# Performance work log

Measured on AMD Instinct MI355X. Metric: run time of the kernel, lower is better.

The kernel has to match this reference:

```python
import jax, jax.numpy as jnp
import numpy as np

B, N, C, H, MC, LIE, KD = 2, 2048, 256, 8, 256, 3, 16
DH = C // H

def swish(x):
    return x * jax.nn.sigmoid(x)

def layernorm(x, g, b):
    m = jnp.mean(x, axis=-1, keepdims=True)
    v = jnp.var(x, axis=-1, keepdims=True)
    return (x - m) * jax.lax.rsqrt(v + 1e-5) * g + b

def setup_inputs():
    ks = jax.random.split(jax.random.key(0), 12)
    p = lambda i, shape, s: jax.random.normal(ks[i], shape, jnp.float32) * s
    return dict(
        pairwise_g=jax.random.normal(ks[0], (B, N, N, LIE), jnp.float32),
        x=jax.random.normal(ks[1], (B, N, C), jnp.float32),
        mask=jnp.ones((B, N), dtype=bool),
        ln1_g=jnp.ones((C,), jnp.float32), ln1_b=jnp.zeros((C,), jnp.float32),
        ln2_g=jnp.ones((C,), jnp.float32), ln2_b=jnp.zeros((C,), jnp.float32),
        wn_w1=p(2, (LIE, KD), 0.3), wn_b1=jnp.zeros((KD,), jnp.float32),
        wn_w2=p(3, (KD, KD), 0.3), wn_b2=jnp.zeros((KD,), jnp.float32),
        wn_w3=p(4, (KD, H), 0.3), wn_b3=jnp.zeros((H,), jnp.float32),
        wq=p(5, (C, C), 0.05), bq=jnp.zeros((C,), jnp.float32),
        wk=p(6, (C, C), 0.05), bk=jnp.zeros((C,), jnp.float32),
        in_w=p(7, (C, C), 0.05), in_b=jnp.zeros((C,), jnp.float32),
        out_w=p(8, (C, C), 0.05), out_b=jnp.zeros((C,), jnp.float32),
        mlp_w1=p(9, (C, C), 0.05), mlp_b1=jnp.zeros((C,), jnp.float32),
        mlp_w2=p(10, (C, C), 0.05), mlp_b2=jnp.zeros((C,), jnp.float32),
    )

def _ema(pairwise_g, x, mask, wn_w1, wn_b1, wn_w2, wn_b2, wn_w3, wn_b3,
         wq, bq, wk, bk, in_w, in_b, out_w, out_b):
    b, n, c = x.shape
    # neighbourhood extraction: topk smallest T(3) group distances (mc_samples=MC, fill=1.0)
    dists = jnp.linalg.norm(pairwise_g, axis=-1)                      # (b,n,n)
    dists = jnp.where(mask[:, None, :], dists, jnp.float32(1e8))
    _, idx = jax.lax.top_k(-dists, MC)                                # (b,n,k)
    nbhd_g = jnp.take_along_axis(pairwise_g, idx[..., None], axis=2)  # (b,n,k,LIE)
    nbhd_mask = jnp.take_along_axis(jnp.broadcast_to(mask[:, None, :], (b, n, n)), idx, axis=2)
    # location kernel: MultiheadWeightNet MLP on pairwise group elements -> per-head scalar
    hloc = swish(nbhd_g @ wn_w1 + wn_b1)
    hloc = swish(hloc @ wn_w2 + wn_b2)
    loc = hloc @ wn_w3 + wn_b3                                        # (b,n,k,H)
    # feature kernel: multihead dot product over gathered neighbour keys
    q = (x @ wq + bq).reshape(b, n, H, DH)
    kf = (x @ wk + bk).reshape(b, n, H, DH)
    k_nbhd = jax.vmap(lambda kfb, ib: kfb[ib])(kf, idx)               # (b,n,k,H,DH)
    scores = jnp.einsum('bnhd,bnkhd->bnkh', q, k_nbhd) / jnp.sqrt(jnp.float32(DH))
    pre = jnp.where(nbhd_mask[..., None], loc + scores, jnp.float32(-1e38))
    attn = jax.nn.softmax(pre, axis=2)                                # (b,n,k,H)
    # values; scatter attention into dense (b,n,n,H) exactly as the torch code, then aggregate
    v = (x @ in_w + in_b).reshape(b, n, H, DH)
    BS = jnp.arange(b)[:, None, None]
    NNS = jnp.arange(n)[None, :, None]
    aw = jnp.zeros((b, n, n, H), attn.dtype).at[BS, NNS, idx].set(attn)
    out = jnp.einsum('bnmh,bmhd->bnhd', aw, v).reshape(b, n, c)
    return out @ out_w + out_b

def reference(pairwise_g, x, mask, ln1_g, ln1_b, ln2_g, ln2_b,
              wn_w1, wn_b1, wn_w2, wn_b2, wn_w3, wn_b3,
              wq, bq, wk, bk, in_w, in_b, out_w, out_b,
              mlp_w1, mlp_b1, mlp_w2, mlp_b2):
    # EquivariantTransformerBlock with block_norm='layer_pre'
    x = x + _ema(pairwise_g, layernorm(x, ln1_g, ln1_b), mask,
                 wn_w1, wn_b1, wn_w2, wn_b2, wn_w3, wn_b3,
                 wq, bq, wk, bk, in_w, in_b, out_w, out_b)
    h = layernorm(x, ln2_g, ln2_b)
    x = x + (swish(h @ mlp_w1 + mlp_b1) @ mlp_w2 + mlp_b2)
    return x
```

## Files before the change

### kernel.cpp

```cpp
#include <hip/hip_runtime.h>
#include <hip/hip_bf16.h>

#define Bb 2
#define Nn 2048
#define Cc 256
#define Hh 8
#define MCk 256
#define RT (Bb * Nn)

typedef __hip_bfloat16 bf16;
typedef _Float16 f16;
typedef __fp16 h2v __attribute__((ext_vector_type(2)));
typedef __fp16 h8 __attribute__((ext_vector_type(8)));
typedef float f32x4 __attribute__((ext_vector_type(4)));
typedef float v2f __attribute__((ext_vector_type(2)));

__device__ __forceinline__ float bl(unsigned u) { return __uint_as_float(u << 16); }
__device__ __forceinline__ float bh(unsigned u) { return __uint_as_float(u & 0xFFFF0000u); }
__device__ __forceinline__ h2v bc16(unsigned u) { return __builtin_bit_cast(h2v, u); }
__device__ __forceinline__ unsigned bcu(h2v v) { return __builtin_bit_cast(unsigned, v); }

__device__ __forceinline__ float dot2(h2v a, h2v b, float c) {
  return __builtin_amdgcn_fdot2(a, b, c, false);
}
__device__ __forceinline__ f32x4 mfma16(h8 a, h8 b, f32x4 c) {
  return __builtin_amdgcn_mfma_f32_16x16x32_f16(a, b, c, 0, 0, 0);
}
__device__ __forceinline__ float swish_f(float z) {
  return z * __builtin_amdgcn_rcpf(1.f + __expf(-z));
}

__global__ __launch_bounds__(256) void prep_w(
    const float* __restrict__ w0, const float* __restrict__ w1,
    const float* __restrict__ w2, const float* __restrict__ w3,
    const float* __restrict__ w4, const float* __restrict__ w5,
    f16* __restrict__ out)
{
  __shared__ float tile[32][33];
  const float* ws_[6] = {w0, w1, w2, w3, w4, w5};
  const float* W = ws_[blockIdx.y];
  f16* o = out + (size_t)blockIdx.y * 65536;
  int tn0 = (blockIdx.x & 7) * 32, tk0 = (blockIdx.x >> 3) * 32;
  int tl = threadIdx.x & 31, tg = threadIdx.x >> 5;
#pragma unroll
  for (int r = 0; r < 4; r++) {
    int k = tk0 + tg * 4 + r;
    tile[tg * 4 + r][tl] = W[(size_t)k * 256 + tn0 + tl];
  }
  __syncthreads();
#pragma unroll
  for (int r = 0; r < 4; r++) {
    int n = tn0 + tg * 4 + r;
    o[(size_t)n * 256 + tk0 + tl] = (f16)tile[tl][tg * 4 + r];
  }
}

__global__ __launch_bounds__(256) void ln_kernel(
    const float* __restrict__ x, const float* __restrict__ g,
    const float* __restrict__ b, f16* __restrict__ out)
{
  int wave = threadIdx.x >> 6, lane = threadIdx.x & 63;
  int row = blockIdx.x * 4 + wave;
  const float4 v = reinterpret_cast<const float4*>(x + (size_t)row * Cc)[lane];
  float s  = v.x + v.y + v.z + v.w;
  float s2 = v.x * v.x + v.y * v.y + v.z * v.z + v.w * v.w;
#pragma unroll
  for (int m = 1; m < 64; m <<= 1) {
    s  += __shfl_xor(s, m);
    s2 += __shfl_xor(s2, m);
  }
  float mean = s * (1.0f / Cc);
  float var  = s2 * (1.0f / Cc) - mean * mean;
  float rs   = rsqrtf(var + 1e-5f);
  const float4 gg = reinterpret_cast<const float4*>(g)[lane];
  const float4 bb = reinterpret_cast<const float4*>(b)[lane];
  float ox = (v.x - mean) * rs * gg.x + bb.x;
  float oy = (v.y - mean) * rs * gg.y + bb.y;
  float oz = (v.z - mean) * rs * gg.z + bb.z;
  float ow = (v.w - mean) * rs * gg.w + bb.w;
  uint2 st;
  st.x = bcu(__builtin_amdgcn_cvt_pkrtz(ox, oy));
  st.y = bcu(__builtin_amdgcn_cvt_pkrtz(oz, ow));
  *(uint2*)(out + (size_t)row * Cc + lane * 4) = st;
}

__global__ __launch_bounds__(256) void gemm_qkv_mfma(
    const f16* __restrict__ A,
    const f16* __restrict__ WTq, const float* __restrict__ Bq,
    const f16* __restrict__ WTk, const float* __restrict__ Bk,
    const f16* __restrict__ WTv, const float* __restrict__ Bv,
    f16* __restrict__ outq, f16* __restrict__ outk, bf16* __restrict__ outv)
{
  int wid = threadIdx.x >> 6, lane = threadIdx.x & 63;
  int m0 = (blockIdx.x * 4 + wid) * 16;
  int n0 = blockIdx.y * 32;
  int lm = lane & 15, lk = lane >> 4;
  const h8* Ab = (const h8*)(A + (size_t)(m0 + lm) * 256) + lk;
  const h8* Q0 = (const h8*)(WTq + (size_t)(n0 + lm) * 256) + lk;
  const h8* Q1 = (const h8*)(WTq + (size_t)(n0 + 16 + lm) * 256) + lk;
  const h8* K0 = (const h8*)(WTk + (size_t)(n0 + lm) * 256) + lk;
  const h8* K1 = (const h8*)(WTk + (size_t)(n0 + 16 + lm) * 256) + lk;
  const h8* V0 = (const h8*)(WTv + (size_t)(n0 + lm) * 256) + lk;
  const h8* V1 = (const h8*)(WTv + (size_t)(n0 + 16 + lm) * 256) + lk;
  f32x4 aq0 = {0.f,0.f,0.f,0.f}, aq1 = {0.f,0.f,0.f,0.f};
  f32x4 ak0 = {0.f,0.f,0.f,0.f}, ak1 = {0.f,0.f,0.f,0.f};
  f32x4 av0 = {0.f,0.f,0.f,0.f}, av1 = {0.f,0.f,0.f,0.f};
#pragma unroll
  for (int ks = 0; ks < 8; ks++) {
    h8 a = Ab[ks * 4];
    aq0 = mfma16(a, Q0[ks * 4], aq0);
    aq1 = mfma16(a, Q1[ks * 4], aq1);
    ak0 = mfma16(a, K0[ks * 4], ak0);
    ak1 = mfma16(a, K1[ks * 4], ak1);
    av0 = mfma16(a, V0[ks * 4], av0);
    av1 = mfma16(a, V1[ks * 4], av1);
  }
  const float qs = 0.17677669529663687f;
  float bq0 = Bq[n0 + lm], bq1 = Bq[n0 + 16 + lm];
  float bk0 = Bk[n0 + lm], bk1 = Bk[n0 + 16 + lm];
  float bv0 = Bv[n0 + lm], bv1 = Bv[n0 + 16 + lm];
#pragma unroll
  for (int i = 0; i < 4; i++) {
    size_t row = m0 + lk * 4 + i;
    outq[row * 256 + n0 + lm]      = (f16)((aq0[i] + bq0) * qs);
    outq[row * 256 + n0 + 16 + lm] = (f16)((aq1[i] + bq1) * qs);
    outk[row * 256 + n0 + lm]      = (f16)(ak0[i] + bk0);
    outk[row * 256 + n0 + 16 + lm] = (f16)(ak1[i] + bk1);
    outv[row * 256 + n0 + lm]      = __float2bfloat16(av0[i] + bv0);
    outv[row * 256 + n0 + 16 + lm] = __float2bfloat16(av1[i] + bv1);
  }
}

__global__ __launch_bounds__(256) void select_kernel(
    const float* __restrict__ pg, int* __restrict__ idxout)
{
  __shared__ int idl[4][256];
  int wave = threadIdx.x >> 6, lane = threadIdx.x & 63;
  int row = blockIdx.x * 4 + wave;
  const float* base = pg + (size_t)row * Nn * 3;
  unsigned u[32];
#pragma unroll
  for (int jj = 0; jj < 32; jj++) {
    int col = jj * 64 + lane;
    float g0 = base[col * 3 + 0];
    float g1 = base[col * 3 + 1];
    float g2 = base[col * 3 + 2];
    u[jj] = __float_as_uint(sqrtf(g0 * g0 + g1 * g1 + g2 * g2));
  }
  unsigned T = 0;
  for (int bit = 30; bit >= 0; bit--) {
    unsigned cand = T | (1u << bit);
    int c = 0;
#pragma unroll
    for (int jj = 0; jj < 32; jj++) c += (u[jj] < cand) ? 1 : 0;
#pragma unroll
    for (int m = 1; m < 64; m <<= 1) c += __shfl_xor(c, m);
    if (c <= MCk - 1) T = cand;
  }
  int cl = 0;
#pragma unroll
  for (int jj = 0; jj < 32; jj++) cl += (u[jj] < T) ? 1 : 0;
#pragma unroll
  for (int m = 1; m < 64; m <<= 1) cl += __shfl_xor(cl, m);
  int need = MCk - cl;
  unsigned long long lmask = (1ull << lane) - 1ull;
  int slot = 0;
  for (int jj = 0; jj < 32; jj++) {
    bool eq = (u[jj] == T);
    unsigned long long em = __ballot(eq);
    int ebelow = __popcll(em & lmask);
    bool sel = (u[jj] < T) || (eq && ebelow < need);
    unsigned long long smsk = __ballot(sel);
    if (sel) idl[wave][slot + __popcll(smsk & lmask)] = jj * 64 + lane;
    slot += __popcll(smsk);
    need -= __popcll(em);
    if (need < 0) need = 0;
  }
#pragma unroll
  for (int s = 0; s < 4; s++)
    idxout[(size_t)row * MCk + s * 64 + lane] = idl[wave][s * 64 + lane];
}

__global__ __launch_bounds__(256) void loc_mlp(
    const float* __restrict__ pg, const int* __restrict__ idxb,
    uint4* __restrict__ locout,
    const float* __restrict__ w1, const float* __restrict__ b1,
    const float* __restrict__ w2, const float* __restrict__ b2,
    const float* __restrict__ w3, const float* __restrict__ b3)
{
  __shared__ float wnl[64];
  __shared__ h2v   w2p[128];
  __shared__ float bn2[16];
  __shared__ h2v   w3p[64];
  __shared__ float bn3[8];
  int t = threadIdx.x;
  int row = blockIdx.x;
  for (int i = t; i < 280; i += 256) {
    if (i < 48) {
      wnl[i] = w1[i];
    } else if (i < 64) {
      wnl[i] = b1[i - 48];
    } else if (i < 192) {
      int j = i - 64, i2 = j >> 4, o = j & 15;
      w2p[j] = __builtin_amdgcn_cvt_pkrtz(w2[(2 * i2) * 16 + o], w2[(2 * i2 + 1) * 16 + o]);
    } else if (i < 208) {
      bn2[i - 192] = b2[i - 192];
    } else if (i < 272) {
      int j = i - 208, i2 = j >> 3, o = j & 7;
      w3p[j] = __builtin_amdgcn_cvt_pkrtz(w3[(2 * i2) * 8 + o], w3[(2 * i2 + 1) * 8 + o]);
    } else {
      bn3[i - 272] = b3[i - 272];
    }
  }
  int m = idxb[(size_t)row * 256 + t];
  const float* gsp = pg + ((size_t)row * Nn + m) * 3;
  float g0 = gsp[0], g1 = gsp[1], g2 = gsp[2];
  __syncthreads();
  float h1[16];
#pragma unroll
  for (int o = 0; o < 16; o++) {
    float z = wnl[48 + o] + g0 * wnl[o] + g1 * wnl[16 + o] + g2 * wnl[32 + o];
    h1[o] = swish_f(z);
  }
  h2v hp1[8];
#pragma unroll
  for (int i = 0; i < 8; i++) hp1[i] = __builtin_amdgcn_cvt_pkrtz(h1[2 * i], h1[2 * i + 1]);
  float hh[16];
#pragma unroll
  for (int o = 0; o < 16; o++) {
    float z = bn2[o];
#pragma unroll
    for (int i2 = 0; i2 < 8; i2++) z = dot2(hp1[i2], w2p[i2 * 16 + o], z);
    hh[o] = swish_f(z);
  }
  h2v hp2[8];
#pragma unroll
  for (int i = 0; i < 8; i++) hp2[i] = __builtin_amdgcn_cvt_pkrtz(hh[2 * i], hh[2 * i + 1]);
  float loc[8];
#pragma unroll
  for (int o = 0; o < 8; o++) {
    float z = bn3[o];
#pragma unroll
    for (int i2 = 0; i2 < 8; i2++) z = dot2(hp2[i2], w3p[i2 * 8 + o], z);
    loc[o] = z;
  }
  uint4 lv;
  lv.x = bcu(__builtin_amdgcn_cvt_pkrtz(loc[0], loc[1]));
  lv.y = bcu(__builtin_amdgcn_cvt_pkrtz(loc[2], loc[3]));
  lv.z = bcu(__builtin_amdgcn_cvt_pkrtz(loc[4], loc[5]));
  lv.w = bcu(__builtin_amdgcn_cvt_pkrtz(loc[6], loc[7]));
  locout[(size_t)row * 256 + t] = lv;
}

__global__ __launch_bounds__(256) void attn_kernel(
    const f16* __restrict__ qh, const f16* __restrict__ kh,
    const bf16* __restrict__ vv, const int* __restrict__ idxb,
    const uint4* __restrict__ loc16, f16* __restrict__ out)
{
  __shared__ int   offs[256];
  __shared__ float ps[256 * 9];
  __shared__ float agg[4 * 256];
  __shared__ float red[4][8];
  int t = threadIdx.x;
  int row = blockIdx.x;
  int bidx = row >> 11;
  int g = t >> 5, c = t & 31;

  int m = idxb[(size_t)row * 256 + t];
  offs[t] = (bidx * Nn + m) * 512;
  const uint4 qu = *(const uint4*)((const char*)qh + (size_t)row * 512 + (size_t)c * 16);
  h2v q0 = bc16(qu.x), q1 = bc16(qu.y), q2 = bc16(qu.z), q3 = bc16(qu.w);
  const uint4 lv = loc16[(size_t)row * 256 + t];
  __syncthreads();

  int offr[32];
#pragma unroll
  for (int kk = 0; kk < 32; kk++) offr[kk] = offs[kk * 8 + g];

  const char* kbase = (const char*)kh;
#pragma unroll
  for (int kk = 0; kk < 32; kk++) {
    const uint4 kv = *(const uint4*)(kbase + offr[kk] + c * 16);
    float p = dot2(bc16(kv.x), q0, 0.f);
    p = dot2(bc16(kv.y), q1, p);
    p = dot2(bc16(kv.z), q2, p);
    p = dot2(bc16(kv.w), q3, p);
    p += __shfl_xor(p, 1);
    p += __shfl_xor(p, 2);
    if ((c & 3) == 0) ps[(kk * 8 + g) * 9 + (c >> 2)] = p;
  }
  __syncthreads();

  h2v l01 = bc16(lv.x), l23 = bc16(lv.y), l45 = bc16(lv.z), l67 = bc16(lv.w);
  float pre[8];
  pre[0] = ps[t * 9 + 0] + (float)l01.x;
  pre[1] = ps[t * 9 + 1] + (float)l01.y;
  pre[2] = ps[t * 9 + 2] + (float)l23.x;
  pre[3] = ps[t * 9 + 3] + (float)l23.y;
  pre[4] = ps[t * 9 + 4] + (float)l45.x;
  pre[5] = ps[t * 9 + 5] + (float)l45.y;
  pre[6] = ps[t * 9 + 6] + (float)l67.x;
  pre[7] = ps[t * 9 + 7] + (float)l67.y;
  float mx[8];
#pragma unroll
  for (int h = 0; h < 8; h++) mx[h] = pre[h];
#pragma unroll
  for (int mm = 1; mm < 64; mm <<= 1) {
#pragma unroll
    for (int h = 0; h < 8; h++) mx[h] = fmaxf(mx[h], __shfl_xor(mx[h], mm));
  }
  int wv = t >> 6, ln = t & 63;
  if (ln == 0) {
#pragma unroll
    for (int h = 0; h < 8; h++) red[wv][h] = mx[h];
  }
  __syncthreads();
#pragma unroll
  for (int h = 0; h < 8; h++)
    mx[h] = fmaxf(fmaxf(red[0][h], red[1][h]), fmaxf(red[2][h], red[3][h]));
  float e[8], sm[8];
#pragma unroll
  for (int h = 0; h < 8; h++) { e[h] = __expf(pre[h] - mx[h]); sm[h] = e[h]; }
  __syncthreads();
#pragma unroll
  for (int mm = 1; mm < 64; mm <<= 1) {
#pragma unroll
    for (int h = 0; h < 8; h++) sm[h] += __shfl_xor(sm[h], mm);
  }
  if (ln == 0) {
#pragma unroll
    for (int h = 0; h < 8; h++) red[wv][h] = sm[h];
  }
  __syncthreads();
#pragma unroll
  for (int h = 0; h < 8; h++) {
    float ssum = red[0][h] + red[1][h] + red[2][h] + red[3][h];
    ps[t * 9 + h] = e[h] * __builtin_amdgcn_rcpf(ssum);
  }
  __syncthreads();

  v2f a01 = {0.f, 0.f}, a23 = {0.f, 0.f}, a45 = {0.f, 0.f}, a67 = {0.f, 0.f};
  const char* vbase = (const char*)vv;
#pragma unroll
  for (int kk = 0; kk < 32; kk++) {
    float aw = ps[(kk * 8 + g) * 9 + (c >> 2)];
    v2f awv = {aw, aw};
    uint4 v4 = *(const uint4*)(vbase + offr[kk] + c * 16);
    v2f p0 = {bl(v4.x), bh(v4.x)};
    v2f p1 = {bl(v4.y), bh(v4.y)};
    v2f p2 = {bl(v4.z), bh(v4.z)};
    v2f p3 = {bl(v4.w), bh(v4.w)};
    a01 = __builtin_elementwise_fma(awv, p0, a01);
    a23 = __builtin_elementwise_fma(awv, p1, a23);
    a45 = __builtin_elementwise_fma(awv, p2, a45);
    a67 = __builtin_elementwise_fma(awv, p3, a67);
  }
  float acc[8] = {a01.x, a01.y, a23.x, a23.y, a45.x, a45.y, a67.x, a67.y};
#pragma unroll
  for (int i = 0; i < 8; i++) acc[i] += __shfl_xor(acc[i], 32);
  if ((t & 32) == 0) {
#pragma unroll
    for (int i = 0; i < 8; i++) agg[wv * 256 + c * 8 + i] = acc[i];
  }
  __syncthreads();
  float o = agg[t] + agg[256 + t] + agg[512 + t] + agg[768 + t];
  out[(size_t)row * 256 + t] = (f16)o;
}

__global__ __launch_bounds__(256) void gemm_out_ln(
    const f16* __restrict__ A, const f16* __restrict__ WT,
    const float* __restrict__ bias, const float* __restrict__ xres,
    const float* __restrict__ g, const float* __restrict__ b,
    float* __restrict__ x1, f16* __restrict__ hout)
{
  __shared__ float sred[4][16][2];
  int wid = threadIdx.x >> 6, lane = threadIdx.x & 63;
  int lm = lane & 15, lk = lane >> 4;
  int m0 = blockIdx.x * 16;
  const h8* Ab = (const h8*)(A + (size_t)(m0 + lm) * 256) + lk;
  const h8* Bp[4];
#pragma unroll
  for (int j = 0; j < 4; j++)
    Bp[j] = (const h8*)(WT + (size_t)(wid * 64 + j * 16 + lm) * 256) + lk;
  f32x4 acc[4] = {{0,0,0,0},{0,0,0,0},{0,0,0,0},{0,0,0,0}};
#pragma unroll
  for (int ks = 0; ks < 8; ks++) {
    h8 a = Ab[ks * 4];
#pragma unroll
    for (int j = 0; j < 4; j++) acc[j] = mfma16(a, Bp[j][ks * 4], acc[j]);
  }
  float s[4] = {0,0,0,0}, s2[4] = {0,0,0,0};
#pragma unroll
  for (int j = 0; j < 4; j++) {
    int col = wid * 64 + j * 16 + lm;
    float bc = bias[col];
#pragma unroll
    for (int i = 0; i < 4; i++) {
      size_t row = m0 + lk * 4 + i;
      float y = acc[j][i] + bc + xres[row * 256 + col];
      acc[j][i] = y;
      x1[row * 256 + col] = y;
      s[i] += y; s2[i] += y * y;
    }
  }
#pragma unroll
  for (int mm = 1; mm < 16; mm <<= 1) {
#pragma unroll
    for (int i = 0; i < 4; i++) {
      s[i]  += __shfl_xor(s[i], mm);
      s2[i] += __shfl_xor(s2[i], mm);
    }
  }
  if (lm == 0) {
#pragma unroll
    for (int i = 0; i < 4; i++) {
      sred[wid][lk * 4 + i][0] = s[i];
      sred[wid][lk * 4 + i][1] = s2[i];
    }
  }
  __syncthreads();
#pragma unroll
  for (int i = 0; i < 4; i++) {
    int r = lk * 4 + i;
    float ts  = sred[0][r][0] + sred[1][r][0] + sred[2][r][0] + sred[3][r][0];
    float ts2 = sred[0][r][1] + sred[1][r][1] + sred[2][r][1] + sred[3][r][1];
    float mean = ts * (1.f / 256.f);
    float var  = ts2 * (1.f / 256.f) - mean * mean;
    float rs   = rsqrtf(var + 1e-5f);
    size_t row = m0 + r;
#pragma unroll
    for (int j = 0; j < 4; j++) {
      int col = wid * 64 + j * 16 + lm;
      float hv = (acc[j][i] - mean) * rs * g[col] + b[col];
      hout[row * 256 + col] = (f16)hv;
    }
  }
}

__global__ __launch_bounds__(256) void mlp_fused(
    const f16* __restrict__ A, const f16* __restrict__ WT1,
    const float* __restrict__ b1, const f16* __restrict__ WT2,
    const float* __restrict__ b2, const float* __restrict__ x1,
    float* __restrict__ outp)
{
  __shared__ f16 hl[16 * 272];
  int wid = threadIdx.x >> 6, lane = threadIdx.x & 63;
  int lm = lane & 15, lk = lane >> 4;
  int m0 = blockIdx.x * 16;
  const h8* Ab = (const h8*)(A + (size_t)(m0 + lm) * 256) + lk;
  const h8* B1p[4];
  const h8* B2p[4];
#pragma unroll
  for (int j = 0; j < 4; j++) {
    B1p[j] = (const h8*)(WT1 + (size_t)(wid * 64 + j * 16 + lm) * 256) + lk;
    B2p[j] = (const h8*)(WT2 + (size_t)(wid * 64 + j * 16 + lm) * 256) + lk;
  }
  f32x4 acc[4] = {{0,0,0,0},{0,0,0,0},{0,0,0,0},{0,0,0,0}};
#pragma unroll
  for (int ks = 0; ks < 8; ks++) {
    h8 a = Ab[ks * 4];
#pragma unroll
    for (int j = 0; j < 4; j++) acc[j] = mfma16(a, B1p[j][ks * 4], acc[j]);
  }
#pragma unroll
  for (int j = 0; j < 4; j++) {
    int col = wid * 64 + j * 16 + lm;
    float bc = b1[col];
#pragma unroll
    for (int i = 0; i < 4; i++) {
      float y = acc[j][i] + bc;
      y = y * __builtin_amdgcn_rcpf(1.f + __expf(-y));
      hl[(lk * 4 + i) * 272 + col] = (f16)y;
    }
  }
  __syncthreads();
  f32x4 ac2[4] = {{0,0,0,0},{0,0,0,0},{0,0,0,0},{0,0,0,0}};
#pragma unroll
  for (int ks = 0; ks < 8; ks++) {
    h8 a2 = *(const h8*)&hl[lm * 272 + ks * 32 + lk * 8];
#pragma unroll
    for (int j = 0; j < 4; j++) ac2[j] = mfma16(a2, B2p[j][ks * 4], ac2[j]);
  }
#pragma unroll
  for (int j = 0; j < 4; j++) {
    int col = wid * 64 + j * 16 + lm;
    float bc = b2[col];
#pragma unroll
    for (int i = 0; i < 4; i++) {
      size_t row = m0 + lk * 4 + i;
      outp[row * 256 + col] = ac2[j][i] + bc + x1[row * 256 + col];
    }
  }
}

extern "C" void kernel_launch(void* const* d_in, const int* in_sizes, int n_in,
                              void* d_out, int out_size, void* d_ws, size_t ws_size,
                              hipStream_t stream)
{
  (void)in_sizes; (void)n_in; (void)out_size; (void)ws_size;
  const float* pg   = (const float*)d_in[0];
  const float* x    = (const float*)d_in[1];
  const float* ln1g = (const float*)d_in[3];
  const float* ln1b = (const float*)d_in[4];
  const float* ln2g = (const float*)d_in[5];
  const float* ln2b = (const float*)d_in[6];
  const float* wnw1 = (const float*)d_in[7];
  const float* wnb1 = (const float*)d_in[8];
  const float* wnw2 = (const float*)d_in[9];
  const float* wnb2 = (const float*)d_in[10];
  const float* wnw3 = (const float*)d_in[11];
  const float* wnb3 = (const float*)d_in[12];
  const float* wq   = (const float*)d_in[13];
  const float* bq   = (const float*)d_in[14];
  const float* wk   = (const float*)d_in[15];
  const float* bk   = (const float*)d_in[16];
  const float* inw  = (const float*)d_in[17];
  const float* inb  = (const float*)d_in[18];
  const float* outw = (const float*)d_in[19];
  const float* outbv= (const float*)d_in[20];
  const float* m1w  = (const float*)d_in[21];
  const float* m1b  = (const float*)d_in[22];
  const float* m2w  = (const float*)d_in[23];
  const float* m2b  = (const float*)d_in[24];

  const size_t RC = (size_t)RT * 256;
  f16*   WTall = (f16*)d_ws;
  f16*   WTq = WTall + 0 * 65536;
  f16*   WTk = WTall + 1 * 65536;
  f16*   WTv = WTall + 2 * 65536;
  f16*   WTo = WTall + 3 * 65536;
  f16*   WTm1= WTall + 4 * 65536;
  f16*   WTm2= WTall + 5 * 65536;
  f16*   ln1h = WTall + 6 * 65536;
  f16*   qh  = ln1h + RC;
  f16*   kh  = qh + RC;
  bf16*  vvb = (bf16*)(kh + RC);
  int*   idxb= (int*)(vvb + RC);
  f16*   emah= (f16*)(idxb + RC);
  void*  R1  = (void*)(emah + RC);
  uint4* loc16 = (uint4*)R1;
  float* x1    = (float*)R1;
  f16*   ln2h  = ln1h;

  dim3 blk(256);
  prep_w<<<dim3(64, 6), blk, 0, stream>>>(wq, wk, inw, outw, m1w, m2w, WTall);
  ln_kernel<<<dim3(RT / 4), blk, 0, stream>>>(x, ln1g, ln1b, ln1h);
  select_kernel<<<dim3(RT / 4), blk, 0, stream>>>(pg, idxb);
  loc_mlp<<<dim3(RT), blk, 0, stream>>>(pg, idxb, loc16,
                                        wnw1, wnb1, wnw2, wnb2, wnw3, wnb3);
  gemm_qkv_mfma<<<dim3(RT / 64, 8), blk, 0, stream>>>(ln1h, WTq, bq, WTk, bk, WTv, inb,
                                                      qh, kh, vvb);
  attn_kernel<<<dim3(RT), blk, 0, stream>>>(qh, kh, vvb, idxb, loc16, emah);
  gemm_out_ln<<<dim3(RT / 16), blk, 0, stream>>>(emah, WTo, outbv, x, ln2g, ln2b,
                                                 x1, ln2h);
  mlp_fused<<<dim3(RT / 16), blk, 0, stream>>>(ln2h, WTm1, m1b, WTm2, m2b, x1,
                                               (float*)d_out);
}
```

Measured before the change: 173.0 us.

## Merge prep and layernorm launches, batch attention loads, widen GEMM blocks

Merges the weight-transpose kernel and the first layernorm into a single launch, so one kernel launch goes away. In the attention kernel, the K and V gathers are batched four at a time to raise memory-level parallelism. Separate reduction buffers let one barrier be removed, and a launch-bounds occupancy hint is added. The out-projection and MLP GEMM kernels move to 512-thread blocks with two column tiles per wave, which spreads the work over more waves but lowers per-wave reuse.

```diff
diff --git a/kernel.cpp b/kernel.cpp
--- a/kernel.cpp
+++ b/kernel.cpp
@@ -30,58 +30,58 @@
   return z * __builtin_amdgcn_rcpf(1.f + __expf(-z));
 }
 
-__global__ __launch_bounds__(256) void prep_w(
+__global__ __launch_bounds__(256) void prep_ln(
     const float* __restrict__ w0, const float* __restrict__ w1,
     const float* __restrict__ w2, const float* __restrict__ w3,
     const float* __restrict__ w4, const float* __restrict__ w5,
-    f16* __restrict__ out)
-{
-  __shared__ float tile[32][33];
-  const float* ws_[6] = {w0, w1, w2, w3, w4, w5};
-  const float* W = ws_[blockIdx.y];
-  f16* o = out + (size_t)blockIdx.y * 65536;
-  int tn0 = (blockIdx.x & 7) * 32, tk0 = (blockIdx.x >> 3) * 32;
-  int tl = threadIdx.x & 31, tg = threadIdx.x >> 5;
-#pragma unroll
-  for (int r = 0; r < 4; r++) {
-    int k = tk0 + tg * 4 + r;
-    tile[tg * 4 + r][tl] = W[(size_t)k * 256 + tn0 + tl];
-  }
-  __syncthreads();
-#pragma unroll
-  for (int r = 0; r < 4; r++) {
-    int n = tn0 + tg * 4 + r;
-    o[(size_t)n * 256 + tk0 + tl] = (f16)tile[tl][tg * 4 + r];
-  }
-}
-
-__global__ __launch_bounds__(256) void ln_kernel(
+    f16* __restrict__ wtout,
     const float* __restrict__ x, const float* __restrict__ g,
-    const float* __restrict__ b, f16* __restrict__ out)
-{
-  int wave = threadIdx.x >> 6, lane = threadIdx.x & 63;
-  int row = blockIdx.x * 4 + wave;
-  const float4 v = reinterpret_cast<const float4*>(x + (size_t)row * Cc)[lane];
-  float s  = v.x + v.y + v.z + v.w;
-  float s2 = v.x * v.x + v.y * v.y + v.z * v.z + v.w * v.w;
-#pragma unroll
-  for (int m = 1; m < 64; m <<= 1) {
-    s  += __shfl_xor(s, m);
-    s2 += __shfl_xor(s2, m);
-  }
-  float mean = s * (1.0f / Cc);
-  float var  = s2 * (1.0f / Cc) - mean * mean;
-  float rs   = rsqrtf(var + 1e-5f);
-  const float4 gg = reinterpret_cast<const float4*>(g)[lane];
-  const float4 bb = reinterpret_cast<const float4*>(b)[lane];
-  float ox = (v.x - mean) * rs * gg.x + bb.x;
-  float oy = (v.y - mean) * rs * gg.y + bb.y;
-  float oz = (v.z - mean) * rs * gg.z + bb.z;
-  float ow = (v.w - mean) * rs * gg.w + bb.w;
-  uint2 st;
-  st.x = bcu(__builtin_amdgcn_cvt_pkrtz(ox, oy));
-  st.y = bcu(__builtin_amdgcn_cvt_pkrtz(oz, ow));
-  *(uint2*)(out + (size_t)row * Cc + lane * 4) = st;
+    const float* __restrict__ b, f16* __restrict__ lnout)
+{
+  if (blockIdx.x < 384) {
+    __shared__ float tile[32][33];
+    int wb = blockIdx.x / 64, tid = blockIdx.x % 64;
+    const float* ws_[6] = {w0, w1, w2, w3, w4, w5};
+    const float* W = ws_[wb];
+    f16* o = wtout + (size_t)wb * 65536;
+    int tn0 = (tid & 7) * 32, tk0 = (tid >> 3) * 32;
+    int tl = threadIdx.x & 31, tg = threadIdx.x >> 5;
+#pragma unroll
+    for (int r = 0; r < 4; r++) {
+      int k = tk0 + tg * 4 + r;
+      tile[tg * 4 + r][tl] = W[(size_t)k * 256 + tn0 + tl];
+    }
+    __syncthreads();
+#pragma unroll
+    for (int r = 0; r < 4; r++) {
+      int n = tn0 + tg * 4 + r;
+      o[(size_t)n * 256 + tk0 + tl] = (f16)tile[tl][tg * 4 + r];
+    }
+  } else {
+    int wave = threadIdx.x >> 6, lane = threadIdx.x & 63;
+    int row = (blockIdx.x - 384) * 4 + wave;
+    const float4 v = reinterpret_cast<const float4*>(x + (size_t)row * Cc)[lane];
+    float s  = v.x + v.y + v.z + v.w;
+    float s2 = v.x * v.x + v.y * v.y + v.z * v.z + v.w * v.w;
+#pragma unroll
+    for (int m = 1; m < 64; m <<= 1) {
+      s  += __shfl_xor(s, m);
+      s2 += __shfl_xor(s2, m);
+    }
+    float mean = s * (1.0f / Cc);
+    float var  = s2 * (1.0f / Cc) - mean * mean;
+    float rs   = rsqrtf(var + 1e-5f);
+    const float4 gg = reinterpret_cast<const float4*>(g)[lane];
+    const float4 bb = reinterpret_cast<const float4*>(b)[lane];
+    float ox = (v.x - mean) * rs * gg.x + bb.x;
+    float oy = (v.y - mean) * rs * gg.y + bb.y;
+    float oz = (v.z - mean) * rs * gg.z + bb.z;
+    float ow = (v.w - mean) * rs * gg.w + bb.w;
+    uint2 st;
+    st.x = bcu(__builtin_amdgcn_cvt_pkrtz(ox, oy));
+    st.y = bcu(__builtin_amdgcn_cvt_pkrtz(oz, ow));
+    *(uint2*)(lnout + (size_t)row * Cc + lane * 4) = st;
+  }
 }
 
 __global__ __launch_bounds__(256) void gemm_qkv_mfma(
@@ -252,7 +252,7 @@
   locout[(size_t)row * 256 + t] = lv;
 }
 
-__global__ __launch_bounds__(256) void attn_kernel(
+__global__ __launch_bounds__(256, 4) void attn_kernel(
     const f16* __restrict__ qh, const f16* __restrict__ kh,
     const bf16* __restrict__ vv, const int* __restrict__ idxb,
     const uint4* __restrict__ loc16, f16* __restrict__ out)
@@ -260,7 +260,8 @@
   __shared__ int   offs[256];
   __shared__ float ps[256 * 9];
   __shared__ float agg[4 * 256];
-  __shared__ float red[4][8];
+  __shared__ float redmx[4][8];
+  __shared__ float redsm[4][8];
   int t = threadIdx.x;
   int row = blockIdx.x;
   int bidx = row >> 11;
@@ -277,17 +278,34 @@
 #pragma unroll
   for (int kk = 0; kk < 32; kk++) offr[kk] = offs[kk * 8 + g];
 
-  const char* kbase = (const char*)kh;
-#pragma unroll
-  for (int kk = 0; kk < 32; kk++) {
-    const uint4 kv = *(const uint4*)(kbase + offr[kk] + c * 16);
-    float p = dot2(bc16(kv.x), q0, 0.f);
-    p = dot2(bc16(kv.y), q1, p);
-    p = dot2(bc16(kv.z), q2, p);
-    p = dot2(bc16(kv.w), q3, p);
-    p += __shfl_xor(p, 1);
-    p += __shfl_xor(p, 2);
-    if ((c & 3) == 0) ps[(kk * 8 + g) * 9 + (c >> 2)] = p;
+  const char* kbase = (const char*)kh + (size_t)c * 16;
+#pragma unroll
+  for (int kk = 0; kk < 32; kk += 4) {
+    const uint4 k0 = *(const uint4*)(kbase + offr[kk + 0]);
+    const uint4 k1 = *(const uint4*)(kbase + offr[kk + 1]);
+    const uint4 k2 = *(const uint4*)(kbase + offr[kk + 2]);
+    const uint4 k3 = *(const uint4*)(kbase + offr[kk + 3]);
+    float p0 = dot2(bc16(k0.x), q0, 0.f);
+    float p1 = dot2(bc16(k1.x), q0, 0.f);
+    float p2 = dot2(bc16(k2.x), q0, 0.f);
+    float p3 = dot2(bc16(k3.x), q0, 0.f);
+    p0 = dot2(bc16(k0.y), q1, p0); p1 = dot2(bc16(k1.y), q1, p1);
+    p2 = dot2(bc16(k2.y), q1, p2); p3 = dot2(bc16(k3.y), q1, p3);
+    p0 = dot2(bc16(k0.z), q2, p0); p1 = dot2(bc16(k1.z), q2, p1);
+    p2 = dot2(bc16(k2.z), q2, p2); p3 = dot2(bc16(k3.z), q2, p3);
+    p0 = dot2(bc16(k0.w), q3, p0); p1 = dot2(bc16(k1.w), q3, p1);
+    p2 = dot2(bc16(k2.w), q3, p2); p3 = dot2(bc16(k3.w), q3, p3);
+    p0 += __shfl_xor(p0, 1); p1 += __shfl_xor(p1, 1);
+    p2 += __shfl_xor(p2, 1); p3 += __shfl_xor(p3, 1);
+    p0 += __shfl_xor(p0, 2); p1 += __shfl_xor(p1, 2);
+    p2 += __shfl_xor(p2, 2); p3 += __shfl_xor(p3, 2);
+    if ((c & 3) == 0) {
+      int hh_ = c >> 2;
+      ps[((kk + 0) * 8 + g) * 9 + hh_] = p0;
+      ps[((kk + 1) * 8 + g) * 9 + hh_] = p1;
+      ps[((kk + 2) * 8 + g) * 9 + hh_] = p2;
+      ps[((kk + 3) * 8 + g) * 9 + hh_] = p3;
+    }
   }
   __syncthreads();
 
@@ -312,16 +330,15 @@
   int wv = t >> 6, ln = t & 63;
   if (ln == 0) {
 #pragma unroll
-    for (int h = 0; h < 8; h++) red[wv][h] = mx[h];
+    for (int h = 0; h < 8; h++) redmx[wv][h] = mx[h];
   }
   __syncthreads();
 #pragma unroll
   for (int h = 0; h < 8; h++)
-    mx[h] = fmaxf(fmaxf(red[0][h], red[1][h]), fmaxf(red[2][h], red[3][h]));
+    mx[h] = fmaxf(fmaxf(redmx[0][h], redmx[1][h]), fmaxf(redmx[2][h], redmx[3][h]));
   float e[8], sm[8];
 #pragma unroll
   for (int h = 0; h < 8; h++) { e[h] = __expf(pre[h] - mx[h]); sm[h] = e[h]; }
-  __syncthreads();
 #pragma unroll
   for (int mm = 1; mm < 64; mm <<= 1) {
 #pragma unroll
@@ -329,31 +346,47 @@
   }
   if (ln == 0) {
 #pragma unroll
-    for (int h = 0; h < 8; h++) red[wv][h] = sm[h];
+    for (int h = 0; h < 8; h++) redsm[wv][h] = sm[h];
   }
   __syncthreads();
 #pragma unroll
   for (int h = 0; h < 8; h++) {
-    float ssum = red[0][h] + red[1][h] + red[2][h] + red[3][h];
+    float ssum = redsm[0][h] + redsm[1][h] + redsm[2][h] + redsm[3][h];
     ps[t * 9 + h] = e[h] * __builtin_amdgcn_rcpf(ssum);
   }
   __syncthreads();
 
   v2f a01 = {0.f, 0.f}, a23 = {0.f, 0.f}, a45 = {0.f, 0.f}, a67 = {0.f, 0.f};
-  const char* vbase = (const char*)vv;
-#pragma unroll
-  for (int kk = 0; kk < 32; kk++) {
-    float aw = ps[(kk * 8 + g) * 9 + (c >> 2)];
-    v2f awv = {aw, aw};
-    uint4 v4 = *(const uint4*)(vbase + offr[kk] + c * 16);
-    v2f p0 = {bl(v4.x), bh(v4.x)};
-    v2f p1 = {bl(v4.y), bh(v4.y)};
-    v2f p2 = {bl(v4.z), bh(v4.z)};
-    v2f p3 = {bl(v4.w), bh(v4.w)};
-    a01 = __builtin_elementwise_fma(awv, p0, a01);
-    a23 = __builtin_elementwise_fma(awv, p1, a23);
-    a45 = __builtin_elementwise_fma(awv, p2, a45);
-    a67 = __builtin_elementwise_fma(awv, p3, a67);
+  const char* vbase = (const char*)vv + (size_t)c * 16;
+  int hh_ = c >> 2;
+#pragma unroll
+  for (int kk = 0; kk < 32; kk += 4) {
+    const uint4 v0 = *(const uint4*)(vbase + offr[kk + 0]);
+    const uint4 v1 = *(const uint4*)(vbase + offr[kk + 1]);
+    const uint4 v2 = *(const uint4*)(vbase + offr[kk + 2]);
+    const uint4 v3 = *(const uint4*)(vbase + offr[kk + 3]);
+    float aw0 = ps[((kk + 0) * 8 + g) * 9 + hh_];
+    float aw1 = ps[((kk + 1) * 8 + g) * 9 + hh_];
+    float aw2 = ps[((kk + 2) * 8 + g) * 9 + hh_];
+    float aw3 = ps[((kk + 3) * 8 + g) * 9 + hh_];
+    v2f w0 = {aw0, aw0}, w1 = {aw1, aw1}, w2 = {aw2, aw2}, w3 = {aw3, aw3};
+    v2f t0, t1, t2, t3;
+    t0 = (v2f){bl(v0.x), bh(v0.x)}; a01 = __builtin_elementwise_fma(w0, t0, a01);
+    t1 = (v2f){bl(v0.y), bh(v0.y)}; a23 = __builtin_elementwise_fma(w0, t1, a23);
+    t2 = (v2f){bl(v0.z), bh(v0.z)}; a45 = __builtin_elementwise_fma(w0, t2, a45);
+    t3 = (v2f){bl(v0.w), bh(v0.w)}; a67 = __builtin_elementwise_fma(w0, t3, a67);
+    t0 = (v2f){bl(v1.x), bh(v1.x)}; a01 = __builtin_elementwise_fma(w1, t0, a01);
+    t1 = (v2f){bl(v1.y), bh(v1.y)}; a23 = __builtin_elementwise_fma(w1, t1, a23);
+    t2 = (v2f){bl(v1.z), bh(v1.z)}; a45 = __builtin_elementwise_fma(w1, t2, a45);
+    t3 = (v2f){bl(v1.w), bh(v1.w)}; a67 = __builtin_elementwise_fma(w1, t3, a67);
+    t0 = (v2f){bl(v2.x), bh(v2.x)}; a01 = __builtin_elementwise_fma(w2, t0, a01);
+    t1 = (v2f){bl(v2.y), bh(v2.y)}; a23 = __builtin_elementwise_fma(w2, t1, a23);
+    t2 = (v2f){bl(v2.z), bh(v2.z)}; a45 = __builtin_elementwise_fma(w2, t2, a45);
+    t3 = (v2f){bl(v2.w), bh(v2.w)}; a67 = __builtin_elementwise_fma(w2, t3, a67);
+    t0 = (v2f){bl(v3.x), bh(v3.x)}; a01 = __builtin_elementwise_fma(w3, t0, a01);
+    t1 = (v2f){bl(v3.y), bh(v3.y)}; a23 = __builtin_elementwise_fma(w3, t1, a23);
+    t2 = (v2f){bl(v3.z), bh(v3.z)}; a45 = __builtin_elementwise_fma(w3, t2, a45);
+    t3 = (v2f){bl(v3.w), bh(v3.w)}; a67 = __builtin_elementwise_fma(w3, t3, a67);
   }
   float acc[8] = {a01.x, a01.y, a23.x, a23.y, a45.x, a45.y, a67.x, a67.y};
 #pragma unroll
@@ -367,41 +400,38 @@
   out[(size_t)row * 256 + t] = (f16)o;
 }
 
-__global__ __launch_bounds__(256) void gemm_out_ln(
+__global__ __launch_bounds__(512) void gemm_out_ln(
     const f16* __restrict__ A, const f16* __restrict__ WT,
     const float* __restrict__ bias, const float* __restrict__ xres,
     const float* __restrict__ g, const float* __restrict__ b,
     float* __restrict__ x1, f16* __restrict__ hout)
 {
-  __shared__ float sred[4][16][2];
+  __shared__ float sred[8][16][2];
   int wid = threadIdx.x >> 6, lane = threadIdx.x & 63;
   int lm = lane & 15, lk = lane >> 4;
   int m0 = blockIdx.x * 16;
   const h8* Ab = (const h8*)(A + (size_t)(m0 + lm) * 256) + lk;
-  const h8* Bp[4];
-#pragma unroll
-  for (int j = 0; j < 4; j++)
-    Bp[j] = (const h8*)(WT + (size_t)(wid * 64 + j * 16 + lm) * 256) + lk;
-  f32x4 acc[4] = {{0,0,0,0},{0,0,0,0},{0,0,0,0},{0,0,0,0}};
+  const h8* Bp0 = (const h8*)(WT + (size_t)(wid * 32 + lm) * 256) + lk;
+  const h8* Bp1 = (const h8*)(WT + (size_t)(wid * 32 + 16 + lm) * 256) + lk;
+  f32x4 ac0 = {0,0,0,0}, ac1 = {0,0,0,0};
 #pragma unroll
   for (int ks = 0; ks < 8; ks++) {
     h8 a = Ab[ks * 4];
-#pragma unroll
-    for (int j = 0; j < 4; j++) acc[j] = mfma16(a, Bp[j][ks * 4], acc[j]);
-  }
-  float s[4] = {0,0,0,0}, s2[4] = {0,0,0,0};
-#pragma unroll
-  for (int j = 0; j < 4; j++) {
-    int col = wid * 64 + j * 16 + lm;
-    float bc = bias[col];
-#pragma unroll
-    for (int i = 0; i < 4; i++) {
-      size_t row = m0 + lk * 4 + i;
-      float y = acc[j][i] + bc + xres[row * 256 + col];
-      acc[j][i] = y;
-      x1[row * 256 + col] = y;
-      s[i] += y; s2[i] += y * y;
-    }
+    ac0 = mfma16(a, Bp0[ks * 4], ac0);
+    ac1 = mfma16(a, Bp1[ks * 4], ac1);
+  }
+  int c0 = wid * 32 + lm, c1 = wid * 32 + 16 + lm;
+  float b0 = bias[c0], b1 = bias[c1];
+  float s[4], s2[4];
+#pragma unroll
+  for (int i = 0; i < 4; i++) {
+    size_t row = m0 + lk * 4 + i;
+    float y0 = ac0[i] + b0 + xres[row * 256 + c0];
+    float y1 = ac1[i] + b1 + xres[row * 256 + c1];
+    ac0[i] = y0; ac1[i] = y1;
+    x1[row * 256 + c0] = y0;
+    x1[row * 256 + c1] = y1;
+    s[i] = y0 + y1; s2[i] = y0 * y0 + y1 * y1;
   }
 #pragma unroll
   for (int mm = 1; mm < 16; mm <<= 1) {
@@ -419,25 +449,23 @@
     }
   }
   __syncthreads();
+  float g0 = g[c0], g1 = g[c1], bb0 = b[c0], bb1 = b[c1];
 #pragma unroll
   for (int i = 0; i < 4; i++) {
     int r = lk * 4 + i;
-    float ts  = sred[0][r][0] + sred[1][r][0] + sred[2][r][0] + sred[3][r][0];
-    float ts2 = sred[0][r][1] + sred[1][r][1] + sred[2][r][1] + sred[3][r][1];
+    float ts = 0.f, ts2 = 0.f;
+#pragma unroll
+    for (int w = 0; w < 8; w++) { ts += sred[w][r][0]; ts2 += sred[w][r][1]; }
     float mean = ts * (1.f / 256.f);
     float var  = ts2 * (1.f / 256.f) - mean * mean;
     float rs   = rsqrtf(var + 1e-5f);
     size_t row = m0 + r;
-#pragma unroll
-    for (int j = 0; j < 4; j++) {
-      int col = wid * 64 + j * 16 + lm;
-      float hv = (acc[j][i] - mean) * rs * g[col] + b[col];
-      hout[row * 256 + col] = (f16)hv;
-    }
-  }
-}
-
-__global__ __launch_bounds__(256) void mlp_fused(
+    hout[row * 256 + c0] = (f16)((ac0[i] - mean) * rs * g0 + bb0);
+    hout[row * 256 + c1] = (f16)((ac1[i] - mean) * rs * g1 + bb1);
+  }
+}
+
+__global__ __launch_bounds__(512) void mlp_fused(
     const f16* __restrict__ A, const f16* __restrict__ WT1,
     const float* __restrict__ b1, const f16* __restrict__ WT2,
     const float* __restrict__ b2, const float* __restrict__ x1,
@@ -448,48 +476,40 @@
   int lm = lane & 15, lk = lane >> 4;
   int m0 = blockIdx.x * 16;
   const h8* Ab = (const h8*)(A + (size_t)(m0 + lm) * 256) + lk;
-  const h8* B1p[4];
-  const h8* B2p[4];
-#pragma unroll
-  for (int j = 0; j < 4; j++) {
-    B1p[j] = (const h8*)(WT1 + (size_t)(wid * 64 + j * 16 + lm) * 256) + lk;
-    B2p[j] = (const h8*)(WT2 + (size_t)(wid * 64 + j * 16 + lm) * 256) + lk;
-  }
-  f32x4 acc[4] = {{0,0,0,0},{0,0,0,0},{0,0,0,0},{0,0,0,0}};
+  const h8* B10 = (const h8*)(WT1 + (size_t)(wid * 32 + lm) * 256) + lk;
+  const h8* B11 = (const h8*)(WT1 + (size_t)(wid * 32 + 16 + lm) * 256) + lk;
+  const h8* B20 = (const h8*)(WT2 + (size_t)(wid * 32 + lm) * 256) + lk;
+  const h8* B21 = (const h8*)(WT2 + (size_t)(wid * 32 + 16 + lm) * 256) + lk;
+  f32x4 ac0 = {0,0,0,0}, ac1 = {0,0,0,0};
 #pragma unroll
   for (int ks = 0; ks < 8; ks++) {
     h8 a = Ab[ks * 4];
-#pragma unroll
-    for (int j = 0; j < 4; j++) acc[j] = mfma16(a, B1p[j][ks * 4], acc[j]);
-  }
-#pragma unroll
-  for (int j = 0; j < 4; j++) {
-    int col = wid * 64 + j * 16 + lm;
-    float bc = b1[col];
-#pragma unroll
-    for (int i = 0; i < 4; i++) {
-      float y = acc[j][i] + bc;
-      y = y * __builtin_amdgcn_rcpf(1.f + __expf(-y));
-      hl[(lk * 4 + i) * 272 + col] = (f16)y;
-    }
-  }
-  __syncthreads();
-  f32x4 ac2[4] = {{0,0,0,0},{0,0,0,0},{0,0,0,0},{0,0,0,0}};
+    ac0 = mfma16(a, B10[ks * 4], ac0);
+    ac1 = mfma16(a, B11[ks * 4], ac1);
+  }
+  int c0 = wid * 32 + lm, c1 = wid * 32 + 16 + lm;
+  float bb0 = b1[c0], bb1 = b1[c1];
+#pragma unroll
+  for (int i = 0; i < 4; i++) {
+    float y0 = ac0[i] + bb0;
+    float y1 = ac1[i] + bb1;
+    hl[(lk * 4 + i) * 272 + c0] = (f16)swish_f(y0);
+    hl[(lk * 4 + i) * 272 + c1] = (f16)swish_f(y1);
+  }
+  __syncthreads();
+  f32x4 o0 = {0,0,0,0}, o1 = {0,0,0,0};
 #pragma unroll
   for (int ks = 0; ks < 8; ks++) {
     h8 a2 = *(const h8*)&hl[lm * 272 + ks * 32 + lk * 8];
-#pragma unroll
-    for (int j = 0; j < 4; j++) ac2[j] = mfma16(a2, B2p[j][ks * 4], ac2[j]);
-  }
-#pragma unroll
-  for (int j = 0; j < 4; j++) {
-    int col = wid * 64 + j * 16 + lm;
-    float bc = b2[col];
-#pragma unroll
-    for (int i = 0; i < 4; i++) {
-      size_t row = m0 + lk * 4 + i;
-      outp[row * 256 + col] = ac2[j][i] + bc + x1[row * 256 + col];
-    }
+    o0 = mfma16(a2, B20[ks * 4], o0);
+    o1 = mfma16(a2, B21[ks * 4], o1);
+  }
+  float d0 = b2[c0], d1 = b2[c1];
+#pragma unroll
+  for (int i = 0; i < 4; i++) {
+    size_t row = m0 + lk * 4 + i;
+    outp[row * 256 + c0] = o0[i] + d0 + x1[row * 256 + c0];
+    outp[row * 256 + c1] = o1[i] + d1 + x1[row * 256 + c1];
   }
 }
 
@@ -543,16 +563,16 @@
   f16*   ln2h  = ln1h;
 
   dim3 blk(256);
-  prep_w<<<dim3(64, 6), blk, 0, stream>>>(wq, wk, inw, outw, m1w, m2w, WTall);
-  ln_kernel<<<dim3(RT / 4), blk, 0, stream>>>(x, ln1g, ln1b, ln1h);
+  prep_ln<<<dim3(384 + RT / 4), blk, 0, stream>>>(wq, wk, inw, outw, m1w, m2w, WTall,
+                                                  x, ln1g, ln1b, ln1h);
   select_kernel<<<dim3(RT / 4), blk, 0, stream>>>(pg, idxb);
   loc_mlp<<<dim3(RT), blk, 0, stream>>>(pg, idxb, loc16,
                                         wnw1, wnb1, wnw2, wnb2, wnw3, wnb3);
   gemm_qkv_mfma<<<dim3(RT / 64, 8), blk, 0, stream>>>(ln1h, WTq, bq, WTk, bk, WTv, inb,
                                                       qh, kh, vvb);
   attn_kernel<<<dim3(RT), blk, 0, stream>>>(qh, kh, vvb, idxb, loc16, emah);
-  gemm_out_ln<<<dim3(RT / 16), blk, 0, stream>>>(emah, WTo, outbv, x, ln2g, ln2b,
-                                                 x1, ln2h);
-  mlp_fused<<<dim3(RT / 16), blk, 0, stream>>>(ln2h, WTm1, m1b, WTm2, m2b, x1,
-                                               (float*)d_out);
-}
+  gemm_out_ln<<<dim3(RT / 16), dim3(512), 0, stream>>>(emah, WTo, outbv, x, ln2g, ln2b,
+                                                       x1, ln2h);
+  mlp_fused<<<dim3(RT / 16), dim3(512), 0, stream>>>(ln2h, WTm1, m1b, WTm2, m2b, x1,
+                                                     (float*)d_out);
+}
```

Measured after the change: 158.4 us. 1.09x faster.
